# Optimization experiments

Measured on AMD Instinct MI355X. Metric: run time of the kernel, lower is better.

## Reference

```python
import jax, jax.numpy as jnp
import numpy as np

N = 20000
E = 600000
D = 512
H = 8
HD = D // H
HID = 1024
FIN = D + 3 * H  # forces_mlp input dim = 536
SCALE = 1.0 / float(np.sqrt(HD))


def _ln(x, g, b, eps=1e-5):
    m = x.mean(-1, keepdims=True)
    v = x.var(-1, keepdims=True)
    return (x - m) / jnp.sqrt(v + eps) * g + b


def _resmlp(h, Wi, bi, Wh, bh, Wo, bo):
    # ResMLP with layers=3: in-proj, one residual hidden block, out-proj
    h = jax.nn.gelu(h @ Wi + bi)
    h = h + jax.nn.gelu(h @ Wh + bh)
    return h @ Wo + bo


def setup_inputs() -> dict:
    key = jax.random.key(0)
    ks = jax.random.split(key, 24)
    s = 0.02
    x = jax.random.normal(ks[0], (N, D), jnp.float32)
    edge_index = jax.random.randint(ks[1], (2, E), 0, N, dtype=jnp.int32)
    att_bias = jax.random.normal(ks[2], (E,), jnp.float32)
    pos = jax.random.normal(ks[3], (N, 3), jnp.float32)
    batch = jnp.zeros((N,), jnp.int32)
    return {
        "x": x, "edge_index": edge_index, "att_bias": att_bias, "pos": pos, "batch": batch,
        "g_att": jnp.ones((D,), jnp.float32), "b_att": jnp.zeros((D,), jnp.float32),
        "g_mlp": jnp.ones((D,), jnp.float32), "b_mlp": jnp.zeros((D,), jnp.float32),
        "Wq": jax.random.normal(ks[4], (D, D), jnp.float32) * s, "bq": jnp.zeros((D,), jnp.float32),
        "Wk": jax.random.normal(ks[5], (D, D), jnp.float32) * s, "bk": jnp.zeros((D,), jnp.float32),
        "We_in": jax.random.normal(ks[6], (D, HID), jnp.float32) * s, "be_in": jnp.zeros((HID,), jnp.float32),
        "We_h": jax.random.normal(ks[7], (HID, HID), jnp.float32) * s, "be_h": jnp.zeros((HID,), jnp.float32),
        "We_out": jax.random.normal(ks[8], (HID, 1), jnp.float32) * s, "be_out": jnp.zeros((1,), jnp.float32),
        "Wf_in": jax.random.normal(ks[9], (FIN, HID), jnp.float32) * s, "bf_in": jnp.zeros((HID,), jnp.float32),
        "Wf_h": jax.random.normal(ks[10], (HID, HID), jnp.float32) * s, "bf_h": jnp.zeros((HID,), jnp.float32),
        "Wf_out": jax.random.normal(ks[11], (HID, 3), jnp.float32) * s, "bf_out": jnp.zeros((3,), jnp.float32),
    }


def reference(x, edge_index, att_bias, pos, batch,
              g_att, b_att, g_mlp, b_mlp, Wq, bq, Wk, bk,
              We_in, be_in, We_h, be_h, We_out, be_out,
              Wf_in, bf_in, Wf_h, bf_h, Wf_out, bf_out):
    n = x.shape[0]
    row, col = edge_index[0], edge_index[1]

    z_att = _ln(x, g_att, b_att)
    q = (z_att @ Wq + bq).reshape(n, H, HD)  # [N,H,HD]
    k = (z_att @ Wk + bk).reshape(n, H, HD)

    # sparse scaled dot product restricted to edges, with additive per-edge bias
    logits = jnp.einsum('ehd,ehd->eh', q[row], k[col]) * SCALE + att_bias[:, None]  # [E,H]
    mx = jax.ops.segment_max(logits, row, num_segments=n)          # [N,H]
    mx = jnp.where(jnp.isfinite(mx), mx, 0.0)
    p = jnp.exp(logits - mx[row])
    denom = jax.ops.segment_sum(p, row, num_segments=n)            # [N,H]
    w = p / denom[row]                                             # [E,H]

    contrib = jnp.einsum('eh,ec->ehc', w, pos[col])                # [E,H,3]
    att = jax.ops.segment_sum(contrib, row, num_segments=n)        # [N,H,3]
    att = att - pos[:, None, :]                                    # att - value
    att = att.reshape(n, H * 3)                                    # permute(1,0,2).view(N,-1)

    z_mlp = _ln(x, g_mlp, b_mlp)
    energy = _resmlp(z_mlp, We_in, be_in, We_h, be_h, We_out, be_out)
    forces = _resmlp(jnp.concatenate([z_mlp, att], axis=-1), Wf_in, bf_in, Wf_h, bf_h, Wf_out, bf_out)
    return (energy, forces)
```

## Files before the change

### kernel.cpp

```cpp
#include <hip/hip_runtime.h>

#define NN 20000
#define EE 600000

typedef unsigned short u16;
typedef unsigned int u32;
typedef float f32x4 __attribute__((ext_vector_type(4)));
typedef u32 u32x4 __attribute__((ext_vector_type(4)));

__device__ __forceinline__ u16 f2bf(float f){
  u32 u = __float_as_uint(f);
  return (u16)((u + 0x7fffu + ((u>>16)&1u))>>16);
}
__device__ __forceinline__ float bf2f(u16 h){ return __uint_as_float(((u32)h)<<16); }

__device__ __forceinline__ float gelu_f(float x){
  float u = 0.7978845608028654f*(x + 0.044715f*x*x*x);
  float e = __expf(2.0f*u);
  return 0.5f*x*(2.0f - 2.0f/(e+1.0f));
}

__global__ __launch_bounds__(256) void ln2_kernel(
    const float* __restrict__ x,
    const float* __restrict__ ga, const float* __restrict__ ba,
    const float* __restrict__ gm, const float* __restrict__ bm,
    u16* __restrict__ za, u16* __restrict__ xf, int N)
{
  int row = (blockIdx.x<<2) + (threadIdx.x>>6);
  int lane = threadIdx.x & 63;
  if(row >= N) return;
  const float* xp = x + ((size_t)row<<9) + (lane<<3);
  f32x4 v0 = *(const f32x4*)xp;
  f32x4 v1 = *(const f32x4*)(xp+4);
  float vals[8] = {v0[0],v0[1],v0[2],v0[3],v1[0],v1[1],v1[2],v1[3]};
  float s=0.f, qs=0.f;
#pragma unroll
  for(int i=0;i<8;i++){ s += vals[i]; qs = fmaf(vals[i],vals[i],qs); }
#pragma unroll
  for(int o=1;o<64;o<<=1){ s += __shfl_xor(s,o); qs += __shfl_xor(qs,o); }
  float mean = s*(1.f/512.f);
  float var  = qs*(1.f/512.f) - mean*mean;
  float rstd = rsqrtf(var + 1e-5f);
  int c0 = lane<<3;
#pragma unroll
  for(int i=0;i<8;i++){
    float zn = (vals[i]-mean)*rstd;
    za[((size_t)row<<9)+c0+i]  = f2bf(fmaf(zn, ga[c0+i], ba[c0+i]));
    xf[(size_t)row*576+c0+i]   = f2bf(fmaf(zn, gm[c0+i], bm[c0+i]));
  }
}

struct WttDesc { const float* W; u16* WT; int K, Nn, Kpad; };
struct WttPack { WttDesc d[6]; };

__global__ __launch_bounds__(256) void wtt_all_kernel(WttPack p)
{
  __shared__ u16 tile[64][65];
  const WttDesc dd = p.d[blockIdx.z];
  const int k0 = blockIdx.x<<6, n0 = blockIdx.y<<6;
  if(k0 >= dd.Kpad || n0 >= dd.Nn) return;
  const int tx = threadIdx.x & 63, ty = threadIdx.x >> 6;
#pragma unroll
  for(int i=0;i<16;i++){
    int r = (i<<2) + ty;
    int gk = k0 + r;
    float v = (gk < dd.K) ? dd.W[(size_t)gk*dd.Nn + n0 + tx] : 0.f;
    tile[r][tx] = f2bf(v);
  }
  __syncthreads();
#pragma unroll
  for(int i=0;i<16;i++){
    int r = (i<<2) + ty;
    dd.WT[(size_t)(n0 + r)*dd.Kpad + k0 + tx] = tile[tx][r];
  }
}

__global__ __launch_bounds__(256) void prep_kernel(
    float* __restrict__ out, const float* __restrict__ beO, const float* __restrict__ bfO,
    float* __restrict__ bqk, const float* __restrict__ bq, const float* __restrict__ bk,
    float* __restrict__ bcat, const float* __restrict__ beI, const float* __restrict__ bfI,
    int* __restrict__ deg)
{
  int idx = blockIdx.x*256 + threadIdx.x;
  if(idx < NN) out[idx] = beO[0];
  else if(idx < NN*4) out[idx] = bfO[(idx - NN) % 3];
  if(idx < 512) bqk[idx] = bq[idx];
  else if(idx < 1024) bqk[idx] = bk[idx-512];
  if(idx < 1024) bcat[idx] = beI[idx];
  else if(idx < 2048) bcat[idx] = bfI[idx-1024];
  if(idx < NN) deg[idx] = 0;
}

__global__ __launch_bounds__(256) void gemm_bt(
    const u16* __restrict__ A, const u16* __restrict__ B,
    const float* __restrict__ bias, const u16* __restrict__ resid,
    u16* __restrict__ Cb, const float* __restrict__ wout,
    float* __restrict__ outp,
    const u16* __restrict__ B2, const float* __restrict__ bias2,
    const float* __restrict__ wout2, float* __restrict__ outp2,
    int M, int N, int K, int lda, int ldr, int mode)
{
  __shared__ u16 As[128*64];
  __shared__ u16 Bs[128*64];
  const int gx = gridDim.x;
  const int b  = blockIdx.y*gx + blockIdx.x;
  const int xcd = b & 7, loc = b >> 3;
  int tileM, tileN, half = 0;
  const u16* Ab = A; const u16* Bp = B; const float* bp = bias;
  if(mode < 2){
    tileM = ((loc/gx)*8 + xcd) << 7;
    tileN = (loc % gx) << 7;
  } else {
    half = xcd >> 2;
    const int mt = ((loc>>3)<<2) + (xcd & 3);
    tileM = mt << 7;
    tileN = (loc & 7) << 7;
    if(half){ Ab = A + 1024; Bp = B2; bp = bias2; }
  }
  if(tileM >= M) return;
  const int tid  = threadIdx.x;
  const int wave = tid>>6, lane = tid&63;
  const int quad = lane>>4, l15 = lane&15;
  const int mhalf = (wave>>1)<<6, nhalf = (wave&1)<<6;
  f32x4 acc[4][4] = {};

  for(int k0=0; k0<K; k0+=64){
#pragma unroll
    for(int j=0;j<4;j++){
      const int c   = (((wave<<2)+j)<<6) + lane;
      const int row = c>>3;
      const int cc  = (c&7) ^ (row&7);
      int gr = tileM + row; gr = (gr < M) ? gr : (M-1);
      const u16* gp = Ab + (size_t)gr*lda + (size_t)(k0 + (cc<<3));
      __builtin_amdgcn_global_load_lds(
        (const __attribute__((address_space(1))) u32*)gp,
        (__attribute__((address_space(3))) u32*)(&As[((wave<<2)+j)<<9]),
        16, 0, 0);
    }
#pragma unroll
    for(int j=0;j<4;j++){
      const int c   = (((wave<<2)+j)<<6) + lane;
      const int row = c>>3;
      const int cc  = (c&7) ^ (row&7);
      const u16* gp = Bp + (size_t)(tileN + row)*K + (size_t)(k0 + (cc<<3));
      __builtin_amdgcn_global_load_lds(
        (const __attribute__((address_space(1))) u32*)gp,
        (__attribute__((address_space(3))) u32*)(&Bs[((wave<<2)+j)<<9]),
        16, 0, 0);
    }
    __syncthreads();
#pragma unroll
    for(int ks=0;ks<2;ks++){
      const int ccol = (ks<<2) + quad;
      u32x4 af[4], bfr[4];
#pragma unroll
      for(int mi=0;mi<4;mi++){
        const int row = mhalf + (mi<<4) + l15;
        af[mi] = *(const u32x4*)&As[((row<<3) + (ccol ^ (row&7)))<<3];
      }
#pragma unroll
      for(int ni=0;ni<4;ni++){
        const int row = nhalf + (ni<<4) + l15;
        bfr[ni] = *(const u32x4*)&Bs[((row<<3) + (ccol ^ (row&7)))<<3];
      }
#pragma unroll
      for(int mi=0;mi<4;mi++)
#pragma unroll
        for(int ni=0;ni<4;ni++)
          asm("v_mfma_f32_16x16x32_bf16 %0, %1, %2, %0"
              : "+v"(acc[mi][ni]) : "v"(af[mi]), "v"(bfr[ni]));
    }
    __syncthreads();
  }

  if(mode <= 1){
#pragma unroll
    for(int mi=0;mi<4;mi++){
#pragma unroll
      for(int reg=0;reg<4;reg++){
        const int gr = tileM + mhalf + (mi<<4) + (quad<<2) + reg;
        if(gr < M){
#pragma unroll
          for(int ni=0;ni<4;ni++){
            const int gc = tileN + nhalf + (ni<<4) + l15;
            float v = acc[mi][ni][reg] + bp[gc];
            if(mode == 1) v = gelu_f(v);
            Cb[(size_t)gr*N + gc] = f2bf(v);
          }
        }
      }
    }
  } else if(!half){
    float wv[4], bv[4];
#pragma unroll
    for(int ni=0;ni<4;ni++){
      int gc = tileN + nhalf + (ni<<4) + l15;
      wv[ni] = wout[gc]; bv[ni] = bp[gc];
    }
#pragma unroll
    for(int mi=0;mi<4;mi++){
#pragma unroll
      for(int reg=0;reg<4;reg++){
        const int gr = tileM + mhalf + (mi<<4) + (quad<<2) + reg;
        if(gr < M){
          float vs = 0.f;
#pragma unroll
          for(int ni=0;ni<4;ni++){
            const int gc = tileN + nhalf + (ni<<4) + l15;
            float v = gelu_f(acc[mi][ni][reg] + bv[ni])
                    + bf2f(resid[(size_t)gr*ldr + gc]);
            vs = fmaf(v, wv[ni], vs);
          }
          vs += __shfl_xor(vs,1); vs += __shfl_xor(vs,2);
          vs += __shfl_xor(vs,4); vs += __shfl_xor(vs,8);
          if(l15 == 0) atomicAdd(&outp[gr], vs);
        }
      }
    }
  } else {
    float wv0[4], wv1[4], wv2[4], bv[4];
#pragma unroll
    for(int ni=0;ni<4;ni++){
      int gc = tileN + nhalf + (ni<<4) + l15;
      wv0[ni] = wout2[gc*3+0]; wv1[ni] = wout2[gc*3+1]; wv2[ni] = wout2[gc*3+2];
      bv[ni] = bp[gc];
    }
#pragma unroll
    for(int mi=0;mi<4;mi++){
#pragma unroll
      for(int reg=0;reg<4;reg++){
        const int gr = tileM + mhalf + (mi<<4) + (quad<<2) + reg;
        if(gr < M){
          float s0=0.f, s1=0.f, s2=0.f;
#pragma unroll
          for(int ni=0;ni<4;ni++){
            const int gc = tileN + nhalf + (ni<<4) + l15;
            float v = gelu_f(acc[mi][ni][reg] + bv[ni])
                    + bf2f(resid[(size_t)gr*ldr + 1024 + gc]);
            s0 = fmaf(v, wv0[ni], s0);
            s1 = fmaf(v, wv1[ni], s1);
            s2 = fmaf(v, wv2[ni], s2);
          }
          s0 += __shfl_xor(s0,1); s0 += __shfl_xor(s0,2); s0 += __shfl_xor(s0,4); s0 += __shfl_xor(s0,8);
          s1 += __shfl_xor(s1,1); s1 += __shfl_xor(s1,2); s1 += __shfl_xor(s1,4); s1 += __shfl_xor(s1,8);
          s2 += __shfl_xor(s2,1); s2 += __shfl_xor(s2,2); s2 += __shfl_xor(s2,4); s2 += __shfl_xor(s2,8);
          if(l15 == 0){
            atomicAdd(&outp2[(size_t)gr*3+0], s0);
            atomicAdd(&outp2[(size_t)gr*3+1], s1);
            atomicAdd(&outp2[(size_t)gr*3+2], s2);
          }
        }
      }
    }
  }
}

__global__ __launch_bounds__(256) void hist_kernel(
    const int* __restrict__ ei, int* __restrict__ deg, int E)
{
  int e = blockIdx.x*256 + threadIdx.x;
  if(e < E) atomicAdd(&deg[ei[e]], 1);
}

__global__ __launch_bounds__(1024) void scan_kernel(
    const int* __restrict__ deg, int* __restrict__ rowptr,
    int* __restrict__ cursor, int N)
{
  __shared__ int wsum[16];
  __shared__ int carry_s;
  const int tid = threadIdx.x, lane = tid & 63, wid = tid >> 6;
  if(tid == 0) carry_s = 0;
  __syncthreads();
  for(int base = 0; base < N; base += 1024){
    int idx = base + tid;
    int v = (idx < N) ? deg[idx] : 0;
    int s = v;
#pragma unroll
    for(int o=1;o<64;o<<=1){ int t = __shfl_up(s,o); if(lane>=o) s += t; }
    if(lane==63) wsum[wid] = s;
    __syncthreads();
    if(wid==0 && lane<16){
      int ws = wsum[lane];
      int t = ws;
#pragma unroll
      for(int o=1;o<16;o<<=1){ int u = __shfl_up(t,o); if(lane>=o) t += u; }
      wsum[lane] = t - ws;
    }
    __syncthreads();
    int ex = s - v + wsum[wid] + carry_s;
    if(idx < N){ rowptr[idx] = ex; cursor[idx] = ex; }
    __syncthreads();
    if(tid == 1023) carry_s += wsum[15] + s;
  }
  __syncthreads();
  if(tid == 0) rowptr[N] = carry_s;
}

__global__ __launch_bounds__(256) void scatter_kernel(
    const int* __restrict__ ei, const float* __restrict__ ab,
    int* __restrict__ cursor, int* __restrict__ cols,
    float* __restrict__ abs_, int E)
{
  int e = blockIdx.x*256 + threadIdx.x;
  if(e >= E) return;
  int r = ei[e];
  int p = atomicAdd(&cursor[r], 1);
  cols[p] = ei[EE + e];
  abs_[p] = ab[e];
}

__global__ __launch_bounds__(256) void node_att_kernel(
    const u16* __restrict__ qk, const int* __restrict__ rowptr,
    const int* __restrict__ cols, const float* __restrict__ abs_,
    const float* __restrict__ pos, u16* __restrict__ xf, int N)
{
  const int node = (blockIdx.x<<2) + (threadIdx.x>>6);
  const int lane = threadIdx.x & 63;
  if(node >= N) return;
  const int h = lane>>3, sub = lane&7;
  const u32x4 qv = *(const u32x4*)(qk + ((size_t)node<<10) + (lane<<3));
  const float posn = (sub<3) ? pos[node*3 + sub] : 0.f;
  const int j1 = rowptr[node+1];
  float den = 0.f, nm = 0.f;

  int j = rowptr[node];
  for(; j+7 < j1; j += 8){
    int c[8]; float abv[8], pv[8]; u32x4 kv[8];
#pragma unroll
    for(int t=0;t<8;t++){ c[t] = cols[j+t]; abv[t] = abs_[j+t]; }
#pragma unroll
    for(int t=0;t<8;t++){
      kv[t] = *(const u32x4*)(qk + ((size_t)c[t]<<10) + 512 + (lane<<3));
      pv[t] = (sub<3) ? pos[c[t]*3+sub] : 0.f;
    }
#pragma unroll
    for(int t=0;t<8;t++){
      float s = 0.f;
#pragma unroll
      for(int i=0;i<4;i++){
        s = fmaf(__uint_as_float(qv[i]<<16),         __uint_as_float(kv[t][i]<<16), s);
        s = fmaf(__uint_as_float(qv[i]&0xffff0000u), __uint_as_float(kv[t][i]&0xffff0000u), s);
      }
      s += __shfl_xor(s,1); s += __shfl_xor(s,2); s += __shfl_xor(s,4);
      float p = __expf(fmaf(s, 0.125f, abv[t]));
      den += p;
      nm = fmaf(p, pv[t], nm);
    }
  }
  for(; j < j1; j++){
    int c0 = cols[j];
    u32x4 kv0 = *(const u32x4*)(qk + ((size_t)c0<<10) + 512 + (lane<<3));
    float pv0 = (sub<3) ? pos[c0*3+sub] : 0.f;
    float s0=0.f;
#pragma unroll
    for(int i=0;i<4;i++){
      s0 = fmaf(__uint_as_float(qv[i]<<16),        __uint_as_float(kv0[i]<<16), s0);
      s0 = fmaf(__uint_as_float(qv[i]&0xffff0000u),__uint_as_float(kv0[i]&0xffff0000u), s0);
    }
    s0 += __shfl_xor(s0,1); s0 += __shfl_xor(s0,2); s0 += __shfl_xor(s0,4);
    float p0 = __expf(fmaf(s0, 0.125f, abs_[j]));
    den += p0;
    nm = fmaf(p0, pv0, nm);
  }

  u16* xp = xf + (size_t)node*576;
  if(sub < 3){
    float a = (den > 0.f) ? nm/den : 0.f;
    xp[512 + h*3 + sub] = f2bf(a - posn);
  } else {
    xp[536 + h*5 + (sub-3)] = 0;
  }
}

extern "C" void kernel_launch(void* const* d_in, const int* in_sizes, int n_in,
                              void* d_out, int out_size, void* d_ws, size_t ws_size,
                              hipStream_t stream)
{
  (void)in_sizes; (void)n_in; (void)out_size; (void)ws_size;
  const float* x    = (const float*)d_in[0];
  const int*   ei   = (const int*)d_in[1];
  const float* ab   = (const float*)d_in[2];
  const float* pos  = (const float*)d_in[3];
  const float* g_att= (const float*)d_in[5];
  const float* b_att= (const float*)d_in[6];
  const float* g_mlp= (const float*)d_in[7];
  const float* b_mlp= (const float*)d_in[8];
  const float* Wq   = (const float*)d_in[9];  const float* bq  = (const float*)d_in[10];
  const float* Wk   = (const float*)d_in[11]; const float* bk  = (const float*)d_in[12];
  const float* WeI  = (const float*)d_in[13]; const float* beI = (const float*)d_in[14];
  const float* WeH  = (const float*)d_in[15]; const float* beH = (const float*)d_in[16];
  const float* WeO  = (const float*)d_in[17]; const float* beO = (const float*)d_in[18];
  const float* WfI  = (const float*)d_in[19]; const float* bfI = (const float*)d_in[20];
  const float* WfH  = (const float*)d_in[21]; const float* bfH = (const float*)d_in[22];
  const float* WfO  = (const float*)d_in[23]; const float* bfO = (const float*)d_in[24];

  char* w = (char*)d_ws;
  size_t off = 0;
  auto alloc = [&](size_t bytes) -> void* {
    void* p = w + off; off += (bytes + 255) & ~(size_t)255; return p;
  };
  u16* zatt  = (u16*)alloc((size_t)NN*512*2);
  u16* qk    = (u16*)alloc((size_t)NN*1024*2);
  u16* xf    = (u16*)alloc((size_t)NN*576*2);
  u16* h1cat = (u16*)alloc((size_t)NN*2048*2);
  u16* wqkT  = (u16*)alloc((size_t)1024*512*2);
  u16* wInT  = (u16*)alloc((size_t)2048*576*2);
  u16* weHT  = (u16*)alloc((size_t)1024*1024*2);
  u16* wfHT  = (u16*)alloc((size_t)1024*1024*2);
  float* bqk    = (float*)alloc((size_t)1024*4);
  float* bcat   = (float*)alloc((size_t)2048*4);
  int*   deg    = (int*)alloc((size_t)NN*4);
  int*   rowptr = (int*)alloc((size_t)(NN+1)*4);
  int*   cursor = (int*)alloc((size_t)NN*4);
  int*   cols   = (int*)alloc((size_t)EE*4);
  float* absrt  = (float*)alloc((size_t)EE*4);

  WttPack pk;
  pk.d[0] = { Wq,  wqkT,            512,  512,  512 };
  pk.d[1] = { Wk,  wqkT + 512*512,  512,  512,  512 };
  pk.d[2] = { WeI, wInT,            512,  1024, 576 };
  pk.d[3] = { WfI, wInT + 1024*576, 536,  1024, 576 };
  pk.d[4] = { WeH, weHT,            1024, 1024, 1024 };
  pk.d[5] = { WfH, wfHT,            1024, 1024, 1024 };
  wtt_all_kernel<<<dim3(16, 16, 6),256,0,stream>>>(pk);

  prep_kernel<<<dim3((NN*4+255)/256),256,0,stream>>>(
      (float*)d_out, beO, bfO, bqk, bq, bk, bcat, beI, bfI, deg);

  ln2_kernel<<<dim3((NN+3)/4),256,0,stream>>>(x, g_att,b_att, g_mlp,b_mlp, zatt, xf, NN);

  hist_kernel   <<<dim3((EE+255)/256),256,0,stream>>>(ei, deg, EE);
  scan_kernel   <<<1,1024,0,stream>>>(deg, rowptr, cursor, NN);
  scatter_kernel<<<dim3((EE+255)/256),256,0,stream>>>(ei, ab, cursor, cols, absrt, EE);

  const int MT = 160;

  gemm_bt<<<dim3(8, MT),256,0,stream>>>(zatt, wqkT, bqk, nullptr, qk,
                                        nullptr, nullptr,
                                        nullptr, nullptr, nullptr, nullptr,
                                        NN, 1024, 512, 512, 0, 0);

  node_att_kernel<<<dim3((NN+3)/4),256,0,stream>>>(qk, rowptr, cols, absrt, pos, xf, NN);

  gemm_bt<<<dim3(16, MT),256,0,stream>>>(xf, wInT, bcat, nullptr, h1cat,
                                         nullptr, nullptr,
                                         nullptr, nullptr, nullptr, nullptr,
                                         NN, 2048, 576, 576, 0, 1);

  gemm_bt<<<dim3(8, 2*MT),256,0,stream>>>(h1cat, weHT, beH, h1cat, nullptr,
                                          WeO, (float*)d_out,
                                          wfHT, bfH, WfO, (float*)d_out + NN,
                                          NN, 1024, 1024, 2048, 2048, 2);
}
```

Measured before the change: 557.5 us.

## Store attention keys in 8-bit float and merge prep kernels into one launch

The QK projection now writes Q in bf16 and K in an 8-bit float format (truncated fp16, 5-bit exponent and 2-bit mantissa). The attention kernel then gathers 8 bytes per lane per edge instead of 16, halving the random-gather traffic of the edge loop. Separately, the weight-transpose, bias-prep, layernorm and degree-histogram kernels are merged into one launch, and degree zeroing moves to a memset. The cost is reduced key precision in the attention logits, which may hurt accuracy, plus extra byte-unpacking ALU work per edge.

```diff
diff --git a/kernel.cpp b/kernel.cpp
--- a/kernel.cpp
+++ b/kernel.cpp
@@ -1,18 +1,31 @@
 #include <hip/hip_runtime.h>
+#include <hip/hip_fp16.h>
 
 #define NN 20000
 #define EE 600000
 
 typedef unsigned short u16;
+typedef unsigned char u8;
 typedef unsigned int u32;
 typedef float f32x4 __attribute__((ext_vector_type(4)));
 typedef u32 u32x4 __attribute__((ext_vector_type(4)));
+typedef u32 u32x2 __attribute__((ext_vector_type(2)));
 
 __device__ __forceinline__ u16 f2bf(float f){
   u32 u = __float_as_uint(f);
   return (u16)((u + 0x7fffu + ((u>>16)&1u))>>16);
 }
 __device__ __forceinline__ float bf2f(u16 h){ return __uint_as_float(((u32)h)<<16); }
+
+__device__ __forceinline__ u8 f2bf8(float v){
+  __half h = __float2half(v);
+  u16 b = *(u16*)&h;
+  return (u8)((b + 0x7Fu + ((b>>8)&1u)) >> 8);
+}
+__device__ __forceinline__ float bf82f(u32 byte){
+  __half_raw r; r.x = (u16)(byte << 8);
+  return __half2float(__half(r));
+}
 
 __device__ __forceinline__ float gelu_f(float x){
   float u = 0.7978845608028654f*(x + 0.044715f*x*x*x);
@@ -20,82 +33,89 @@
   return 0.5f*x*(2.0f - 2.0f/(e+1.0f));
 }
 
-__global__ __launch_bounds__(256) void ln2_kernel(
+struct WttDesc { const float* W; u16* WT; int K, Nn, Kpad; };
+struct WttPack { WttDesc d[6]; };
+
+#define B_WTT  1536
+#define B_PREP 313
+#define B_LN2  5000
+#define B_HIST 2344
+
+__global__ __launch_bounds__(256) void misc_kernel(
+    WttPack p,
+    float* __restrict__ out, const float* __restrict__ beO, const float* __restrict__ bfO,
+    float* __restrict__ bqk, const float* __restrict__ bq, const float* __restrict__ bk,
+    float* __restrict__ bcat, const float* __restrict__ beI, const float* __restrict__ bfI,
     const float* __restrict__ x,
     const float* __restrict__ ga, const float* __restrict__ ba,
     const float* __restrict__ gm, const float* __restrict__ bm,
-    u16* __restrict__ za, u16* __restrict__ xf, int N)
-{
-  int row = (blockIdx.x<<2) + (threadIdx.x>>6);
-  int lane = threadIdx.x & 63;
-  if(row >= N) return;
-  const float* xp = x + ((size_t)row<<9) + (lane<<3);
-  f32x4 v0 = *(const f32x4*)xp;
-  f32x4 v1 = *(const f32x4*)(xp+4);
-  float vals[8] = {v0[0],v0[1],v0[2],v0[3],v1[0],v1[1],v1[2],v1[3]};
-  float s=0.f, qs=0.f;
-#pragma unroll
-  for(int i=0;i<8;i++){ s += vals[i]; qs = fmaf(vals[i],vals[i],qs); }
-#pragma unroll
-  for(int o=1;o<64;o<<=1){ s += __shfl_xor(s,o); qs += __shfl_xor(qs,o); }
-  float mean = s*(1.f/512.f);
-  float var  = qs*(1.f/512.f) - mean*mean;
-  float rstd = rsqrtf(var + 1e-5f);
-  int c0 = lane<<3;
-#pragma unroll
-  for(int i=0;i<8;i++){
-    float zn = (vals[i]-mean)*rstd;
-    za[((size_t)row<<9)+c0+i]  = f2bf(fmaf(zn, ga[c0+i], ba[c0+i]));
-    xf[(size_t)row*576+c0+i]   = f2bf(fmaf(zn, gm[c0+i], bm[c0+i]));
-  }
-}
-
-struct WttDesc { const float* W; u16* WT; int K, Nn, Kpad; };
-struct WttPack { WttDesc d[6]; };
-
-__global__ __launch_bounds__(256) void wtt_all_kernel(WttPack p)
+    u16* __restrict__ za, u16* __restrict__ xf,
+    const int* __restrict__ ei, int* __restrict__ deg)
 {
   __shared__ u16 tile[64][65];
-  const WttDesc dd = p.d[blockIdx.z];
-  const int k0 = blockIdx.x<<6, n0 = blockIdx.y<<6;
-  if(k0 >= dd.Kpad || n0 >= dd.Nn) return;
-  const int tx = threadIdx.x & 63, ty = threadIdx.x >> 6;
-#pragma unroll
-  for(int i=0;i<16;i++){
-    int r = (i<<2) + ty;
-    int gk = k0 + r;
-    float v = (gk < dd.K) ? dd.W[(size_t)gk*dd.Nn + n0 + tx] : 0.f;
-    tile[r][tx] = f2bf(v);
-  }
-  __syncthreads();
-#pragma unroll
-  for(int i=0;i<16;i++){
-    int r = (i<<2) + ty;
-    dd.WT[(size_t)(n0 + r)*dd.Kpad + k0 + tx] = tile[tx][r];
-  }
-}
-
-__global__ __launch_bounds__(256) void prep_kernel(
-    float* __restrict__ out, const float* __restrict__ beO, const float* __restrict__ bfO,
-    float* __restrict__ bqk, const float* __restrict__ bq, const float* __restrict__ bk,
-    float* __restrict__ bcat, const float* __restrict__ beI, const float* __restrict__ bfI,
-    int* __restrict__ deg)
-{
-  int idx = blockIdx.x*256 + threadIdx.x;
-  if(idx < NN) out[idx] = beO[0];
-  else if(idx < NN*4) out[idx] = bfO[(idx - NN) % 3];
-  if(idx < 512) bqk[idx] = bq[idx];
-  else if(idx < 1024) bqk[idx] = bk[idx-512];
-  if(idx < 1024) bcat[idx] = beI[idx];
-  else if(idx < 2048) bcat[idx] = bfI[idx-1024];
-  if(idx < NN) deg[idx] = 0;
+  const int b = blockIdx.x;
+  const int tid = threadIdx.x;
+  if(b < B_WTT){
+    const WttDesc dd = p.d[b >> 8];
+    const int r8 = b & 255;
+    const int k0 = (r8 & 15) << 6, n0 = (r8 >> 4) << 6;
+    if(k0 >= dd.Kpad || n0 >= dd.Nn) return;
+    const int tx = tid & 63, ty = tid >> 6;
+#pragma unroll
+    for(int i=0;i<16;i++){
+      int r = (i<<2) + ty;
+      int gk = k0 + r;
+      float v = (gk < dd.K) ? dd.W[(size_t)gk*dd.Nn + n0 + tx] : 0.f;
+      tile[r][tx] = f2bf(v);
+    }
+    __syncthreads();
+#pragma unroll
+    for(int i=0;i<16;i++){
+      int r = (i<<2) + ty;
+      dd.WT[(size_t)(n0 + r)*dd.Kpad + k0 + tx] = tile[tx][r];
+    }
+  } else if(b < B_WTT + B_PREP){
+    int idx = (b - B_WTT)*256 + tid;
+    if(idx < NN) out[idx] = beO[0];
+    else if(idx < NN*4) out[idx] = bfO[(idx - NN) % 3];
+    if(idx < 512) bqk[idx] = bq[idx];
+    else if(idx < 1024) bqk[idx] = bk[idx-512];
+    if(idx < 1024) bcat[idx] = beI[idx];
+    else if(idx < 2048) bcat[idx] = bfI[idx-1024];
+  } else if(b < B_WTT + B_PREP + B_LN2){
+    int row = ((b - B_WTT - B_PREP)<<2) + (tid>>6);
+    int lane = tid & 63;
+    if(row >= NN) return;
+    const float* xp = x + ((size_t)row<<9) + (lane<<3);
+    f32x4 v0 = *(const f32x4*)xp;
+    f32x4 v1 = *(const f32x4*)(xp+4);
+    float vals[8] = {v0[0],v0[1],v0[2],v0[3],v1[0],v1[1],v1[2],v1[3]};
+    float s=0.f, qs=0.f;
+#pragma unroll
+    for(int i=0;i<8;i++){ s += vals[i]; qs = fmaf(vals[i],vals[i],qs); }
+#pragma unroll
+    for(int o=1;o<64;o<<=1){ s += __shfl_xor(s,o); qs += __shfl_xor(qs,o); }
+    float mean = s*(1.f/512.f);
+    float var  = qs*(1.f/512.f) - mean*mean;
+    float rstd = rsqrtf(var + 1e-5f);
+    int c0 = lane<<3;
+#pragma unroll
+    for(int i=0;i<8;i++){
+      float zn = (vals[i]-mean)*rstd;
+      za[((size_t)row<<9)+c0+i] = f2bf(fmaf(zn, ga[c0+i], ba[c0+i]));
+      xf[(size_t)row*576+c0+i]  = f2bf(fmaf(zn, gm[c0+i], bm[c0+i]));
+    }
+  } else {
+    int e = (b - B_WTT - B_PREP - B_LN2)*256 + tid;
+    if(e < EE) atomicAdd(&deg[ei[e]], 1);
+  }
 }
 
 __global__ __launch_bounds__(256) void gemm_bt(
     const u16* __restrict__ A, const u16* __restrict__ B,
     const float* __restrict__ bias, const u16* __restrict__ resid,
-    u16* __restrict__ Cb, const float* __restrict__ wout,
-    float* __restrict__ outp,
+    u16* __restrict__ Cb, u8* __restrict__ k8,
+    const float* __restrict__ wout, float* __restrict__ outp,
     const u16* __restrict__ B2, const float* __restrict__ bias2,
     const float* __restrict__ wout2, float* __restrict__ outp2,
     int M, int N, int K, int lda, int ldr, int mode)
@@ -173,7 +193,7 @@
     __syncthreads();
   }
 
-  if(mode <= 1){
+  if(mode == 0){
 #pragma unroll
     for(int mi=0;mi<4;mi++){
 #pragma unroll
@@ -184,8 +204,23 @@
           for(int ni=0;ni<4;ni++){
             const int gc = tileN + nhalf + (ni<<4) + l15;
             float v = acc[mi][ni][reg] + bp[gc];
-            if(mode == 1) v = gelu_f(v);
-            Cb[(size_t)gr*N + gc] = f2bf(v);
+            if(gc < 512) Cb[(size_t)gr*512 + gc] = f2bf(v);
+            else         k8[(size_t)gr*512 + gc - 512] = f2bf8(v);
+          }
+        }
+      }
+    }
+  } else if(mode == 1){
+#pragma unroll
+    for(int mi=0;mi<4;mi++){
+#pragma unroll
+      for(int reg=0;reg<4;reg++){
+        const int gr = tileM + mhalf + (mi<<4) + (quad<<2) + reg;
+        if(gr < M){
+#pragma unroll
+          for(int ni=0;ni<4;ni++){
+            const int gc = tileN + nhalf + (ni<<4) + l15;
+            Cb[(size_t)gr*N + gc] = f2bf(gelu_f(acc[mi][ni][reg] + bp[gc]));
           }
         }
       }
@@ -255,13 +290,6 @@
   }
 }
 
-__global__ __launch_bounds__(256) void hist_kernel(
-    const int* __restrict__ ei, int* __restrict__ deg, int E)
-{
-  int e = blockIdx.x*256 + threadIdx.x;
-  if(e < E) atomicAdd(&deg[ei[e]], 1);
-}
-
 __global__ __launch_bounds__(1024) void scan_kernel(
     const int* __restrict__ deg, int* __restrict__ rowptr,
     int* __restrict__ cursor, int N)
@@ -310,36 +338,43 @@
 }
 
 __global__ __launch_bounds__(256) void node_att_kernel(
-    const u16* __restrict__ qk, const int* __restrict__ rowptr,
-    const int* __restrict__ cols, const float* __restrict__ abs_,
-    const float* __restrict__ pos, u16* __restrict__ xf, int N)
+    const u16* __restrict__ qd, const u8* __restrict__ k8,
+    const int* __restrict__ rowptr, const int* __restrict__ cols,
+    const float* __restrict__ abs_, const float* __restrict__ pos,
+    u16* __restrict__ xf, int N)
 {
   const int node = (blockIdx.x<<2) + (threadIdx.x>>6);
   const int lane = threadIdx.x & 63;
   if(node >= N) return;
   const int h = lane>>3, sub = lane&7;
-  const u32x4 qv = *(const u32x4*)(qk + ((size_t)node<<10) + (lane<<3));
+  const u32x4 qv = *(const u32x4*)(qd + ((size_t)node<<9) + (lane<<3));
+  float qf[8];
+#pragma unroll
+  for(int i=0;i<4;i++){
+    qf[2*i]   = __uint_as_float(qv[i]<<16);
+    qf[2*i+1] = __uint_as_float(qv[i]&0xffff0000u);
+  }
   const float posn = (sub<3) ? pos[node*3 + sub] : 0.f;
   const int j1 = rowptr[node+1];
   float den = 0.f, nm = 0.f;
 
   int j = rowptr[node];
   for(; j+7 < j1; j += 8){
-    int c[8]; float abv[8], pv[8]; u32x4 kv[8];
+    int c[8]; float abv[8], pv[8]; u32x2 kw[8];
 #pragma unroll
     for(int t=0;t<8;t++){ c[t] = cols[j+t]; abv[t] = abs_[j+t]; }
 #pragma unroll
     for(int t=0;t<8;t++){
-      kv[t] = *(const u32x4*)(qk + ((size_t)c[t]<<10) + 512 + (lane<<3));
+      kw[t] = *(const u32x2*)(k8 + ((size_t)c[t]<<9) + (lane<<3));
       pv[t] = (sub<3) ? pos[c[t]*3+sub] : 0.f;
     }
 #pragma unroll
     for(int t=0;t<8;t++){
       float s = 0.f;
 #pragma unroll
-      for(int i=0;i<4;i++){
-        s = fmaf(__uint_as_float(qv[i]<<16),         __uint_as_float(kv[t][i]<<16), s);
-        s = fmaf(__uint_as_float(qv[i]&0xffff0000u), __uint_as_float(kv[t][i]&0xffff0000u), s);
+      for(int i=0;i<8;i++){
+        u32 byte = (kw[t][i>>2] >> ((i&3)<<3)) & 0xFFu;
+        s = fmaf(qf[i], bf82f(byte), s);
       }
       s += __shfl_xor(s,1); s += __shfl_xor(s,2); s += __shfl_xor(s,4);
       float p = __expf(fmaf(s, 0.125f, abv[t]));
@@ -349,13 +384,13 @@
   }
   for(; j < j1; j++){
     int c0 = cols[j];
-    u32x4 kv0 = *(const u32x4*)(qk + ((size_t)c0<<10) + 512 + (lane<<3));
+    u32x2 kw0 = *(const u32x2*)(k8 + ((size_t)c0<<9) + (lane<<3));
     float pv0 = (sub<3) ? pos[c0*3+sub] : 0.f;
     float s0=0.f;
 #pragma unroll
-    for(int i=0;i<4;i++){
-      s0 = fmaf(__uint_as_float(qv[i]<<16),        __uint_as_float(kv0[i]<<16), s0);
-      s0 = fmaf(__uint_as_float(qv[i]&0xffff0000u),__uint_as_float(kv0[i]&0xffff0000u), s0);
+    for(int i=0;i<8;i++){
+      u32 byte = (kw0[i>>2] >> ((i&3)<<3)) & 0xFFu;
+      s0 = fmaf(qf[i], bf82f(byte), s0);
     }
     s0 += __shfl_xor(s0,1); s0 += __shfl_xor(s0,2); s0 += __shfl_xor(s0,4);
     float p0 = __expf(fmaf(s0, 0.125f, abs_[j]));
@@ -400,7 +435,8 @@
     void* p = w + off; off += (bytes + 255) & ~(size_t)255; return p;
   };
   u16* zatt  = (u16*)alloc((size_t)NN*512*2);
-  u16* qk    = (u16*)alloc((size_t)NN*1024*2);
+  u16* qd    = (u16*)alloc((size_t)NN*512*2);
+  u8*  k8    = (u8*) alloc((size_t)NN*512);
   u16* xf    = (u16*)alloc((size_t)NN*576*2);
   u16* h1cat = (u16*)alloc((size_t)NN*2048*2);
   u16* wqkT  = (u16*)alloc((size_t)1024*512*2);
@@ -415,6 +451,8 @@
   int*   cols   = (int*)alloc((size_t)EE*4);
   float* absrt  = (float*)alloc((size_t)EE*4);
 
+  hipMemsetAsync(deg, 0, (size_t)NN*4, stream);
+
   WttPack pk;
   pk.d[0] = { Wq,  wqkT,            512,  512,  512 };
   pk.d[1] = { Wk,  wqkT + 512*512,  512,  512,  512 };
@@ -422,32 +460,28 @@
   pk.d[3] = { WfI, wInT + 1024*576, 536,  1024, 576 };
   pk.d[4] = { WeH, weHT,            1024, 1024, 1024 };
   pk.d[5] = { WfH, wfHT,            1024, 1024, 1024 };
-  wtt_all_kernel<<<dim3(16, 16, 6),256,0,stream>>>(pk);
-
-  prep_kernel<<<dim3((NN*4+255)/256),256,0,stream>>>(
-      (float*)d_out, beO, bfO, bqk, bq, bk, bcat, beI, bfI, deg);
-
-  ln2_kernel<<<dim3((NN+3)/4),256,0,stream>>>(x, g_att,b_att, g_mlp,b_mlp, zatt, xf, NN);
-
-  hist_kernel   <<<dim3((EE+255)/256),256,0,stream>>>(ei, deg, EE);
+  misc_kernel<<<dim3(B_WTT+B_PREP+B_LN2+B_HIST),256,0,stream>>>(
+      pk, (float*)d_out, beO, bfO, bqk, bq, bk, bcat, beI, bfI,
+      x, g_att, b_att, g_mlp, b_mlp, zatt, xf, ei, deg);
+
   scan_kernel   <<<1,1024,0,stream>>>(deg, rowptr, cursor, NN);
   scatter_kernel<<<dim3((EE+255)/256),256,0,stream>>>(ei, ab, cursor, cols, absrt, EE);
 
   const int MT = 160;
 
-  gemm_bt<<<dim3(8, MT),256,0,stream>>>(zatt, wqkT, bqk, nullptr, qk,
+  gemm_bt<<<dim3(8, MT),256,0,stream>>>(zatt, wqkT, bqk, nullptr, qd, k8,
                                         nullptr, nullptr,
                                         nullptr, nullptr, nullptr, nullptr,
                                         NN, 1024, 512, 512, 0, 0);
 
-  node_att_kernel<<<dim3((NN+3)/4),256,0,stream>>>(qk, rowptr, cols, absrt, pos, xf, NN);
-
-  gemm_bt<<<dim3(16, MT),256,0,stream>>>(xf, wInT, bcat, nullptr, h1cat,
+  node_att_kernel<<<dim3((NN+3)/4),256,0,stream>>>(qd, k8, rowptr, cols, absrt, pos, xf, NN);
+
+  gemm_bt<<<dim3(16, MT),256,0,stream>>>(xf, wInT, bcat, nullptr, h1cat, nullptr,
                                          nullptr, nullptr,
                                          nullptr, nullptr, nullptr, nullptr,
                                          NN, 2048, 576, 576, 0, 1);
 
-  gemm_bt<<<dim3(8, 2*MT),256,0,stream>>>(h1cat, weHT, beH, h1cat, nullptr,
+  gemm_bt<<<dim3(8, 2*MT),256,0,stream>>>(h1cat, weHT, beH, h1cat, nullptr, nullptr,
                                           WeO, (float*)d_out,
                                           wfHT, bfH, WfO, (float*)d_out + NN,
                                           NN, 1024, 1024, 2048, 2048, 2);
```

After: 513.6 us. 7.9% less time.
